# Kernel tuning notes

Hardware: AMD Instinct MI355X
Metric: run time of the kernel (lower is better)

## Reference

```python
import jax, jax.numpy as jnp
import numpy as np

# ---- static forest structure: 1024 complete binary trees of depth 9 ----
N_TREES = 1024
DEPTH = 9
NPT = 2 ** (DEPTH + 1) - 1            # 1023 nodes per tree
DIM = N_TREES * NPT                    # 1,047,552 total nodes
C = 10                                 # hidden states
M = 128                                # emission alphabet
N_GEN = 4                              # parallel generative models
LEVEL_SIZES = [N_TREES * 2 ** (k + 1) for k in range(DEPTH)]
LEVEL_START = np.concatenate([[0], np.cumsum(LEVEL_SIZES)]).astype(np.int64)
TREE_OFF = np.arange(N_TREES, dtype=np.int64) * NPT


def _build_forest():
    parents, children = [], []
    for k in range(DEPTH):
        ch = np.arange(2 ** (k + 1) - 1, 2 ** (k + 2) - 1, dtype=np.int64)  # depth k+1 nodes
        pa = (ch - 1) // 2                                                   # their parents (depth k)
        children.append((TREE_OFF[:, None] + ch[None, :]).ravel())
        parents.append((TREE_OFF[:, None] + pa[None, :]).ravel())
    leaves = (TREE_OFF[:, None] + np.arange(NPT // 2, NPT, dtype=np.int64)[None, :]).ravel()
    trees_ind = np.repeat(np.arange(N_TREES, dtype=np.int64), NPT)
    return np.concatenate(parents), np.concatenate(children), leaves, trees_ind


def setup_inputs() -> dict:
    key = jax.random.key(0)
    k1, k2, k3, k4 = jax.random.split(key, 4)
    parents, children, leaves, trees_ind = _build_forest()
    return {
        "x": jax.random.randint(k4, (DIM,), 0, M, dtype=jnp.int32),
        "A": jax.random.normal(k1, (C, C, N_GEN), jnp.float32) * 2.5,
        "B": jax.random.normal(k2, (C, M, N_GEN), jnp.float32) * 2.5,
        "Pi": jax.random.normal(k3, (C, N_GEN), jnp.float32) * 2.5,
        "parents": jnp.asarray(parents, jnp.int32),
        "children": jnp.asarray(children, jnp.int32),
        "trees_ind": jnp.asarray(trees_ind, jnp.int32),
        "leaves": jnp.asarray(leaves, jnp.int32),
    }


def _upward(x, A, B, Pi, parents, children, trees_ind, leaves):
    # softmax reparameterization (vectorized over the n_gen axis)
    smA = jax.nn.softmax(A, axis=0)    # P(parent state i | child state j), cols sum over i
    smB = jax.nn.softmax(B, axis=1)    # emission distribution per state
    smPi = jax.nn.softmax(Pi, axis=0)  # leaf prior

    beta = jnp.zeros((DIM, C, N_GEN), smA.dtype)
    t_beta = jnp.zeros((DIM, C, N_GEN), smA.dtype)
    ll = jnp.zeros((DIM, N_GEN), smA.dtype)

    # leaves: beta = Pi * B[:, x_leaf], normalized
    B_leaf = jnp.swapaxes(smB[:, x[leaves]], 0, 1)            # [L, C, G]
    b = smPi[None, :, :] * B_leaf
    nu = b.sum(axis=1)                                         # [L, G]
    beta = beta.at[leaves].set(b / nu[:, None, :])
    ll = ll.at[leaves].set(jnp.log(nu))

    # bottom-up sweep over levels (static loop over tree depth)
    for k in reversed(range(DEPTH)):
        s, e = int(LEVEL_START[k]), int(LEVEL_START[k + 1])
        pa, ch = parents[s:e], children[s:e]
        beta_ch = beta[ch]                                     # [E, C, G]
        tb_ch = jnp.einsum('ijg,ejg->eig', smA, beta_ch)       # sum over child state j
        sums = jax.ops.segment_sum(tb_ch, pa, num_segments=DIM)
        cnt = jax.ops.segment_sum(jnp.ones((e - s,), smA.dtype), pa, num_segments=DIM)
        t_beta = t_beta + sums / jnp.maximum(cnt, 1.0)[:, None, None]  # scatter-mean over children
        # unique parents at this level = all depth-k nodes (static for complete trees)
        u = jnp.asarray((TREE_OFF[:, None] + np.arange(2 ** k - 1, 2 ** (k + 1) - 1)[None, :]).ravel(), jnp.int32)
        B_u = jnp.swapaxes(smB[:, x[u]], 0, 1)                 # [U, C, G]
        bl = t_beta[u] * B_u
        nu = bl.sum(axis=1)
        beta = beta.at[u].set(bl / nu[:, None, :])
        ll = ll.at[u].set(jnp.log(nu))

    # per-tree log-likelihood: scatter-sum node terms over trees_ind
    return jax.ops.segment_sum(ll, trees_ind, num_segments=N_TREES)  # [n_trees, G]


def reference(x, A, B, Pi, parents, children, trees_ind, leaves):
    return _upward(x, A, B, Pi, parents, children, trees_ind, leaves)
```

## Files before the change

### kernel.cpp

```cpp
#include <hip/hip_runtime.h>
#include <math.h>

#define NC     10
#define NCP    12
#define NM     128
#define NGEN   4
#define NPT    1023
#define NTREES 1024

#define RCPF(x) __builtin_amdgcn_rcpf(x)
#define WAVE_FENCE() __builtin_amdgcn_wave_barrier()

struct F12 { float4 a, b, c; };

__device__ __forceinline__ F12 ld12(const float* p) {
    F12 r; const float4* q = (const float4*)p;
    r.a = q[0]; r.b = q[1]; r.c = q[2]; return r;
}
__device__ __forceinline__ void unpack10(float* t, const F12& r) {
    t[0] = r.a.x; t[1] = r.a.y; t[2] = r.a.z; t[3] = r.a.w;
    t[4] = r.b.x; t[5] = r.b.y; t[6] = r.b.z; t[7] = r.b.w;
    t[8] = r.c.x; t[9] = r.c.y;
}
__device__ __forceinline__ void fma10(float* t, const F12& c, float s) {
    t[0] += c.a.x * s; t[1] += c.a.y * s; t[2] += c.a.z * s; t[3] += c.a.w * s;
    t[4] += c.b.x * s; t[5] += c.b.y * s; t[6] += c.b.z * s; t[7] += c.b.w * s;
    t[8] += c.c.x * s; t[9] += c.c.y * s;
}
__device__ __forceinline__ void mul10(float* t, const F12& r) {
    t[0] *= r.a.x; t[1] *= r.a.y; t[2] *= r.a.z; t[3] *= r.a.w;
    t[4] *= r.b.x; t[5] *= r.b.y; t[6] *= r.b.z; t[7] *= r.b.w;
    t[8] *= r.c.x; t[9] *= r.c.y;
}
__device__ __forceinline__ float sum10(const float* v) {
    return (((v[0] + v[1]) + (v[2] + v[3])) + ((v[4] + v[5]) + (v[6] + v[7]))) + (v[8] + v[9]);
}

__device__ __forceinline__ float leaf_pair(const float (*sBTpi)[NCP], int xv0, int xv1, float* sc) {
    float b0[NC], b1[NC];
    unpack10(b0, ld12(&sBTpi[xv0][0]));
    unpack10(b1, ld12(&sBTpi[xv1][0]));
    const float nu0 = sum10(b0), nu1 = sum10(b1);
    const float r0 = RCPF(nu0), r1 = RCPF(nu1);
    #pragma unroll
    for (int j = 0; j < NC; ++j) sc[j] = b0[j] * r0 + b1[j] * r1;
    return __logf(nu0) + __logf(nu1);
}

__device__ __forceinline__ float node_step(const F12* acol, const float (*sBT)[NCP],
                                           const float* sc, int xv, float* bout) {
    float t[NC];
    #pragma unroll
    for (int i = 0; i < NC; ++i) t[i] = 0.f;
    #pragma unroll
    for (int j = 0; j < NC; ++j) fma10(t, acol[j], sc[j]);
    mul10(t, ld12(&sBT[xv][0]));
    const float nu = sum10(t);
    const float r = RCPF(nu);
    #pragma unroll
    for (int j = 0; j < NC; ++j) bout[j] = t[j] * r;
    return __logf(nu);
}

__device__ __forceinline__ float fused_step_ip(const F12* acol, const float (*sBT)[NCP],
                                               float* buf, int l,
                                               int xc0, int xc1, int xp)
{
    float t0[NC], t1[NC];
    #pragma unroll
    for (int i = 0; i < NC; ++i) { t0[i] = 0.f; t1[i] = 0.f; }
    #pragma unroll
    for (int j = 0; j < NC; ++j) {
        float4 gv = *(const float4*)(buf + j * 64 + 4 * l);
        fma10(t0, acol[j], gv.x + gv.y);
        fma10(t1, acol[j], gv.z + gv.w);
    }
    mul10(t0, ld12(&sBT[xc0][0]));
    mul10(t1, ld12(&sBT[xc1][0]));
    const float nu0 = sum10(t0), nu1 = sum10(t1);
    const float r0 = RCPF(nu0), r1 = RCPF(nu1);
    float ll = __logf(nu0) + __logf(nu1);

    float tp[NC];
    #pragma unroll
    for (int i = 0; i < NC; ++i) tp[i] = 0.f;
    #pragma unroll
    for (int j = 0; j < NC; ++j)
        fma10(tp, acol[j], t0[j] * r0 + t1[j] * r1);
    mul10(tp, ld12(&sBT[xp][0]));
    const float nup = sum10(tp);
    ll += __logf(nup);
    const float rp = RCPF(nup);
    #pragma unroll
    for (int j = 0; j < NC; ++j) buf[j * 64 + l] = tp[j] * rp;
    return ll;
}

__global__ __launch_bounds__(256)
void htmm_fused(const int* __restrict__ x,
                const float* __restrict__ A,
                const float* __restrict__ B,
                const float* __restrict__ Pi,
                float* __restrict__ out)
{
    __shared__ __align__(16) float sACol[NC][NCP];
    __shared__ __align__(16) float sBT[NM][NCP];
    __shared__ __align__(16) float sBTpi[NM][NCP];
    __shared__ __align__(16) float sPiP[NCP];
    __shared__ __align__(16) float sB6[4][NC][64];

    const int bid = blockIdx.x;
    const int g = bid >> 8;
    const int treeBase = (bid & 255) * 4;
    const int tid = threadIdx.x;
    const int u = tid >> 6, lane = tid & 63;

    {
        for (int c = u; c < NC; c += 4) {
            float v0 = B[(c * NM + lane) * NGEN + g];
            float v1 = B[(c * NM + lane + 64) * NGEN + g];
            float mx = fmaxf(v0, v1);
            #pragma unroll
            for (int off = 32; off; off >>= 1) mx = fmaxf(mx, __shfl_xor(mx, off));
            float e0 = __expf(v0 - mx), e1 = __expf(v1 - mx);
            float s = e0 + e1;
            #pragma unroll
            for (int off = 32; off; off >>= 1) s += __shfl_xor(s, off);
            float rs = 1.f / s;
            sBT[lane][c]      = e0 * rs;
            sBT[lane + 64][c] = e1 * rs;
        }
        if (tid < NC) {
            const int j = tid;
            float col[NC], mx = -1e30f;
            #pragma unroll
            for (int i = 0; i < NC; ++i) { col[i] = A[(i * NC + j) * NGEN + g]; mx = fmaxf(mx, col[i]); }
            float s = 0.f;
            #pragma unroll
            for (int i = 0; i < NC; ++i) { col[i] = __expf(col[i] - mx); s += col[i]; }
            const float rs = 0.5f / s;
            #pragma unroll
            for (int i = 0; i < NC; ++i) sACol[j][i] = col[i] * rs;
            sACol[j][10] = 0.f; sACol[j][11] = 0.f;
        }
        if (tid == 16) {
            float col[NC], mx = -1e30f;
            #pragma unroll
            for (int i = 0; i < NC; ++i) { col[i] = Pi[i * NGEN + g]; mx = fmaxf(mx, col[i]); }
            float s = 0.f;
            #pragma unroll
            for (int i = 0; i < NC; ++i) { col[i] = __expf(col[i] - mx); s += col[i]; }
            const float rs = 1.f / s;
            #pragma unroll
            for (int i = 0; i < NC; ++i) sPiP[i] = col[i] * rs;
            sPiP[10] = 0.f; sPiP[11] = 0.f;
        }
    }
    __syncthreads();
    if (tid < NM) {
        F12 pi = ld12(sPiP);
        F12 r  = ld12(&sBT[tid][0]);
        sBTpi[tid][0] = pi.a.x * r.a.x; sBTpi[tid][1] = pi.a.y * r.a.y;
        sBTpi[tid][2] = pi.a.z * r.a.z; sBTpi[tid][3] = pi.a.w * r.a.w;
        sBTpi[tid][4] = pi.b.x * r.b.x; sBTpi[tid][5] = pi.b.y * r.b.y;
        sBTpi[tid][6] = pi.b.z * r.b.z; sBTpi[tid][7] = pi.b.w * r.b.w;
        sBTpi[tid][8] = pi.c.x * r.c.x; sBTpi[tid][9] = pi.c.y * r.c.y;
    }
    __syncthreads();

    F12 acol[NC];
    #pragma unroll
    for (int j = 0; j < NC; ++j) acol[j] = ld12(&sACol[j][0]);

    const int tree = treeBase + u;
    const int tb = tree * NPT;
    const int s = lane;

    int xl[8];
    #pragma unroll
    for (int k = 0; k < 8; ++k) xl[k] = x[tb + 511 + 8 * s + k];
    int x8v[4];
    #pragma unroll
    for (int c = 0; c < 4; ++c) x8v[c] = x[tb + 255 + 4 * s + c];
    const int x7a = x[tb + 127 + 2 * s];
    const int x7b = x[tb + 128 + 2 * s];
    const int x6v = x[tb + 63 + s];

    float llacc = 0.f;
    float sc[NC], ba[NC], bb[NC], b7a[NC], b7b[NC];

    llacc += leaf_pair(sBTpi, xl[0], xl[1], sc);
    llacc += node_step(acol, sBT, sc, x8v[0], ba);
    llacc += leaf_pair(sBTpi, xl[2], xl[3], sc);
    llacc += node_step(acol, sBT, sc, x8v[1], bb);
    #pragma unroll
    for (int j = 0; j < NC; ++j) sc[j] = ba[j] + bb[j];
    llacc += node_step(acol, sBT, sc, x7a, b7a);

    llacc += leaf_pair(sBTpi, xl[4], xl[5], sc);
    llacc += node_step(acol, sBT, sc, x8v[2], ba);
    llacc += leaf_pair(sBTpi, xl[6], xl[7], sc);
    llacc += node_step(acol, sBT, sc, x8v[3], bb);
    #pragma unroll
    for (int j = 0; j < NC; ++j) sc[j] = ba[j] + bb[j];
    llacc += node_step(acol, sBT, sc, x7b, b7b);

    #pragma unroll
    for (int j = 0; j < NC; ++j) sc[j] = b7a[j] + b7b[j];
    llacc += node_step(acol, sBT, sc, x6v, ba);
    #pragma unroll
    for (int j = 0; j < NC; ++j) sB6[u][j][s] = ba[j];

    WAVE_FENCE();
    float lla = 0.f;
    if (lane < 16)
        lla = fused_step_ip(acol, sBT, &sB6[u][0][0], lane,
                            x[tb + 31 + 2 * lane], x[tb + 32 + 2 * lane],
                            x[tb + 15 + lane]);
    llacc += lla;
    WAVE_FENCE();
    float llb = 0.f;
    if (lane < 4)
        llb = fused_step_ip(acol, sBT, &sB6[u][0][0], lane,
                            x[tb + 7 + 2 * lane], x[tb + 8 + 2 * lane],
                            x[tb + 3 + lane]);
    llacc += llb;
    WAVE_FENCE();
    if (lane == 0)
        llacc += fused_step_ip(acol, sBT, &sB6[u][0][0], 0,
                               x[tb + 1], x[tb + 2], x[tb + 0]);

    #pragma unroll
    for (int off = 32; off; off >>= 1) llacc += __shfl_down(llacc, off);
    if (lane == 0) out[tree * NGEN + g] = llacc;
}

extern "C" void kernel_launch(void* const* d_in, const int* in_sizes, int n_in,
                              void* d_out, int out_size, void* d_ws, size_t ws_size,
                              hipStream_t stream) {
    const int*   x  = (const int*)d_in[0];
    const float* A  = (const float*)d_in[1];
    const float* B  = (const float*)d_in[2];
    const float* Pi = (const float*)d_in[3];
    float* out = (float*)d_out;
    htmm_fused<<<NTREES, 256, 0, stream>>>(x, A, B, Pi, out);
}
```

Before: 28.65 us.

## Split softmax table setup into separate kernel and read tables from global memory

Adds a small setup kernel that computes the softmaxed A, B and Pi-weighted B tables once per generative model into workspace memory. The main kernel then launches one 64-thread block per (tree, model) and reads the tables from global memory through cache, no longer rebuilding them in LDS inside every block. This is meant to remove the per-block table construction and its block barrier. In exchange it adds a second launch and scattered global/L2 gathers where LDS reads were used before. The old fused kernel stays as a fallback when the workspace is too small.

```diff
diff --git a/kernel.cpp b/kernel.cpp
--- a/kernel.cpp
+++ b/kernel.cpp
@@ -8,6 +8,11 @@
 #define NPT    1023
 #define NTREES 1024
 
+#define WS_BT(g)    ((g) * (NM * NCP))
+#define WS_BTPI(g)  (4 * NM * NCP + (g) * (NM * NCP))
+#define WS_AC(g)    (8 * NM * NCP + (g) * (NC * NCP))
+#define WS_FLOATS   (8 * NM * NCP + 4 * NC * NCP)
+
 #define RCPF(x) __builtin_amdgcn_rcpf(x)
 #define WAVE_FENCE() __builtin_amdgcn_wave_barrier()
 
@@ -36,10 +41,10 @@
     return (((v[0] + v[1]) + (v[2] + v[3])) + ((v[4] + v[5]) + (v[6] + v[7]))) + (v[8] + v[9]);
 }
 
-__device__ __forceinline__ float leaf_pair(const float (*sBTpi)[NCP], int xv0, int xv1, float* sc) {
+__device__ __forceinline__ float leaf_pair(const float* btpi, int xv0, int xv1, float* sc) {
     float b0[NC], b1[NC];
-    unpack10(b0, ld12(&sBTpi[xv0][0]));
-    unpack10(b1, ld12(&sBTpi[xv1][0]));
+    unpack10(b0, ld12(btpi + NCP * xv0));
+    unpack10(b1, ld12(btpi + NCP * xv1));
     const float nu0 = sum10(b0), nu1 = sum10(b1);
     const float r0 = RCPF(nu0), r1 = RCPF(nu1);
     #pragma unroll
@@ -47,14 +52,14 @@
     return __logf(nu0) + __logf(nu1);
 }
 
-__device__ __forceinline__ float node_step(const F12* acol, const float (*sBT)[NCP],
+__device__ __forceinline__ float node_step(const F12* acol, const float* bt,
                                            const float* sc, int xv, float* bout) {
     float t[NC];
     #pragma unroll
     for (int i = 0; i < NC; ++i) t[i] = 0.f;
     #pragma unroll
     for (int j = 0; j < NC; ++j) fma10(t, acol[j], sc[j]);
-    mul10(t, ld12(&sBT[xv][0]));
+    mul10(t, ld12(bt + NCP * xv));
     const float nu = sum10(t);
     const float r = RCPF(nu);
     #pragma unroll
@@ -62,7 +67,7 @@
     return __logf(nu);
 }
 
-__device__ __forceinline__ float fused_step_ip(const F12* acol, const float (*sBT)[NCP],
+__device__ __forceinline__ float fused_step_ip(const F12* acol, const float* bt,
                                                float* buf, int l,
                                                int xc0, int xc1, int xp)
 {
@@ -75,8 +80,8 @@
         fma10(t0, acol[j], gv.x + gv.y);
         fma10(t1, acol[j], gv.z + gv.w);
     }
-    mul10(t0, ld12(&sBT[xc0][0]));
-    mul10(t1, ld12(&sBT[xc1][0]));
+    mul10(t0, ld12(bt + NCP * xc0));
+    mul10(t1, ld12(bt + NCP * xc1));
     const float nu0 = sum10(t0), nu1 = sum10(t1);
     const float r0 = RCPF(nu0), r1 = RCPF(nu1);
     float ll = __logf(nu0) + __logf(nu1);
@@ -87,13 +92,158 @@
     #pragma unroll
     for (int j = 0; j < NC; ++j)
         fma10(tp, acol[j], t0[j] * r0 + t1[j] * r1);
-    mul10(tp, ld12(&sBT[xp][0]));
+    mul10(tp, ld12(bt + NCP * xp));
     const float nup = sum10(tp);
     ll += __logf(nup);
     const float rp = RCPF(nup);
     #pragma unroll
     for (int j = 0; j < NC; ++j) buf[j * 64 + l] = tp[j] * rp;
     return ll;
+}
+
+__global__ __launch_bounds__(256)
+void htmm_setup(const float* __restrict__ A,
+                const float* __restrict__ B,
+                const float* __restrict__ Pi,
+                float* __restrict__ ws)
+{
+    __shared__ float sPi[NCP];
+    const int g = blockIdx.x;
+    const int tid = threadIdx.x;
+    const int wave = tid >> 6, lane = tid & 63;
+    float* bt   = ws + WS_BT(g);
+    float* btpi = ws + WS_BTPI(g);
+    float* ac   = ws + WS_AC(g);
+
+    if (tid == 16) {
+        float col[NC], mx = -1e30f;
+        #pragma unroll
+        for (int i = 0; i < NC; ++i) { col[i] = Pi[i * NGEN + g]; mx = fmaxf(mx, col[i]); }
+        float s = 0.f;
+        #pragma unroll
+        for (int i = 0; i < NC; ++i) { col[i] = __expf(col[i] - mx); s += col[i]; }
+        const float rs = 1.f / s;
+        #pragma unroll
+        for (int i = 0; i < NC; ++i) sPi[i] = col[i] * rs;
+    }
+    if (tid < NC) {
+        const int j = tid;
+        float col[NC], mx = -1e30f;
+        #pragma unroll
+        for (int i = 0; i < NC; ++i) { col[i] = A[(i * NC + j) * NGEN + g]; mx = fmaxf(mx, col[i]); }
+        float s = 0.f;
+        #pragma unroll
+        for (int i = 0; i < NC; ++i) { col[i] = __expf(col[i] - mx); s += col[i]; }
+        const float rs = 0.5f / s;
+        #pragma unroll
+        for (int i = 0; i < NC; ++i) ac[j * NCP + i] = col[i] * rs;
+        ac[j * NCP + 10] = 0.f; ac[j * NCP + 11] = 0.f;
+    }
+    __syncthreads();
+
+    for (int c = wave; c < NC; c += 4) {
+        float v0 = B[(c * NM + lane) * NGEN + g];
+        float v1 = B[(c * NM + lane + 64) * NGEN + g];
+        float mx = fmaxf(v0, v1);
+        #pragma unroll
+        for (int off = 32; off; off >>= 1) mx = fmaxf(mx, __shfl_xor(mx, off));
+        float e0 = __expf(v0 - mx), e1 = __expf(v1 - mx);
+        float s = e0 + e1;
+        #pragma unroll
+        for (int off = 32; off; off >>= 1) s += __shfl_xor(s, off);
+        const float rs = 1.f / s;
+        const float pic = sPi[c];
+        bt[lane * NCP + c]          = e0 * rs;
+        bt[(lane + 64) * NCP + c]   = e1 * rs;
+        btpi[lane * NCP + c]        = e0 * rs * pic;
+        btpi[(lane + 64) * NCP + c] = e1 * rs * pic;
+    }
+    if (tid < NM) {
+        bt[tid * NCP + 10] = 0.f;   bt[tid * NCP + 11] = 0.f;
+        btpi[tid * NCP + 10] = 0.f; btpi[tid * NCP + 11] = 0.f;
+    }
+}
+
+__global__ __launch_bounds__(64)
+void htmm_main(const int* __restrict__ x,
+               const float* __restrict__ ws,
+               float* __restrict__ out)
+{
+    __shared__ __align__(16) float sB6[NC][64];
+
+    const int bid  = blockIdx.x;
+    const int tree = bid >> 2;
+    const int g    = bid & 3;
+    const int lane = threadIdx.x;
+
+    const float* bt   = ws + WS_BT(g);
+    const float* btpi = ws + WS_BTPI(g);
+    const float* ac   = ws + WS_AC(g);
+
+    F12 acol[NC];
+    #pragma unroll
+    for (int j = 0; j < NC; ++j) acol[j] = ld12(ac + j * NCP);
+
+    const int tb = tree * NPT;
+    const int s = lane;
+
+    int xl[8];
+    #pragma unroll
+    for (int k = 0; k < 8; ++k) xl[k] = x[tb + 511 + 8 * s + k];
+    int x8v[4];
+    #pragma unroll
+    for (int c = 0; c < 4; ++c) x8v[c] = x[tb + 255 + 4 * s + c];
+    const int x7a = x[tb + 127 + 2 * s];
+    const int x7b = x[tb + 128 + 2 * s];
+    const int x6v = x[tb + 63 + s];
+
+    float llacc = 0.f;
+    float sc[NC], ba[NC], bb[NC], b7a[NC], b7b[NC];
+
+    llacc += leaf_pair(btpi, xl[0], xl[1], sc);
+    llacc += node_step(acol, bt, sc, x8v[0], ba);
+    llacc += leaf_pair(btpi, xl[2], xl[3], sc);
+    llacc += node_step(acol, bt, sc, x8v[1], bb);
+    #pragma unroll
+    for (int j = 0; j < NC; ++j) sc[j] = ba[j] + bb[j];
+    llacc += node_step(acol, bt, sc, x7a, b7a);
+
+    llacc += leaf_pair(btpi, xl[4], xl[5], sc);
+    llacc += node_step(acol, bt, sc, x8v[2], ba);
+    llacc += leaf_pair(btpi, xl[6], xl[7], sc);
+    llacc += node_step(acol, bt, sc, x8v[3], bb);
+    #pragma unroll
+    for (int j = 0; j < NC; ++j) sc[j] = ba[j] + bb[j];
+    llacc += node_step(acol, bt, sc, x7b, b7b);
+
+    #pragma unroll
+    for (int j = 0; j < NC; ++j) sc[j] = b7a[j] + b7b[j];
+    llacc += node_step(acol, bt, sc, x6v, ba);
+    #pragma unroll
+    for (int j = 0; j < NC; ++j) sB6[j][s] = ba[j];
+
+    WAVE_FENCE();
+    float lla = 0.f;
+    if (lane < 16)
+        lla = fused_step_ip(acol, bt, &sB6[0][0], lane,
+                            x[tb + 31 + 2 * lane], x[tb + 32 + 2 * lane],
+                            x[tb + 15 + lane]);
+    llacc += lla;
+    WAVE_FENCE();
+    float llb = 0.f;
+    if (lane < 4)
+        llb = fused_step_ip(acol, bt, &sB6[0][0], lane,
+                            x[tb + 7 + 2 * lane], x[tb + 8 + 2 * lane],
+                            x[tb + 3 + lane]);
+    llacc += llb;
+    WAVE_FENCE();
+    if (lane == 0)
+        llacc += fused_step_ip(acol, bt, &sB6[0][0], 0,
+                               x[tb + 1], x[tb + 2], x[tb + 0]);
+
+    #pragma unroll
+    for (int off = 32; off; off >>= 1) llacc += __shfl_down(llacc, off);
+    if (lane == 0) out[tree * NGEN + g] = llacc;
 }
 
 __global__ __launch_bounds__(256)
@@ -189,45 +339,45 @@
     float llacc = 0.f;
     float sc[NC], ba[NC], bb[NC], b7a[NC], b7b[NC];
 
-    llacc += leaf_pair(sBTpi, xl[0], xl[1], sc);
-    llacc += node_step(acol, sBT, sc, x8v[0], ba);
-    llacc += leaf_pair(sBTpi, xl[2], xl[3], sc);
-    llacc += node_step(acol, sBT, sc, x8v[1], bb);
+    llacc += leaf_pair(&sBTpi[0][0], xl[0], xl[1], sc);
+    llacc += node_step(acol, &sBT[0][0], sc, x8v[0], ba);
+    llacc += leaf_pair(&sBTpi[0][0], xl[2], xl[3], sc);
+    llacc += node_step(acol, &sBT[0][0], sc, x8v[1], bb);
     #pragma unroll
     for (int j = 0; j < NC; ++j) sc[j] = ba[j] + bb[j];
-    llacc += node_step(acol, sBT, sc, x7a, b7a);
-
-    llacc += leaf_pair(sBTpi, xl[4], xl[5], sc);
-    llacc += node_step(acol, sBT, sc, x8v[2], ba);
-    llacc += leaf_pair(sBTpi, xl[6], xl[7], sc);
-    llacc += node_step(acol, sBT, sc, x8v[3], bb);
+    llacc += node_step(acol, &sBT[0][0], sc, x7a, b7a);
+
+    llacc += leaf_pair(&sBTpi[0][0], xl[4], xl[5], sc);
+    llacc += node_step(acol, &sBT[0][0], sc, x8v[2], ba);
+    llacc += leaf_pair(&sBTpi[0][0], xl[6], xl[7], sc);
+    llacc += node_step(acol, &sBT[0][0], sc, x8v[3], bb);
     #pragma unroll
     for (int j = 0; j < NC; ++j) sc[j] = ba[j] + bb[j];
-    llacc += node_step(acol, sBT, sc, x7b, b7b);
+    llacc += node_step(acol, &sBT[0][0], sc, x7b, b7b);
 
     #pragma unroll
     for (int j = 0; j < NC; ++j) sc[j] = b7a[j] + b7b[j];
-    llacc += node_step(acol, sBT, sc, x6v, ba);
+    llacc += node_step(acol, &sBT[0][0], sc, x6v, ba);
     #pragma unroll
     for (int j = 0; j < NC; ++j) sB6[u][j][s] = ba[j];
 
     WAVE_FENCE();
     float lla = 0.f;
     if (lane < 16)
-        lla = fused_step_ip(acol, sBT, &sB6[u][0][0], lane,
+        lla = fused_step_ip(acol, &sBT[0][0], &sB6[u][0][0], lane,
                             x[tb + 31 + 2 * lane], x[tb + 32 + 2 * lane],
                             x[tb + 15 + lane]);
     llacc += lla;
     WAVE_FENCE();
     float llb = 0.f;
     if (lane < 4)
-        llb = fused_step_ip(acol, sBT, &sB6[u][0][0], lane,
+        llb = fused_step_ip(acol, &sBT[0][0], &sB6[u][0][0], lane,
                             x[tb + 7 + 2 * lane], x[tb + 8 + 2 * lane],
                             x[tb + 3 + lane]);
     llacc += llb;
     WAVE_FENCE();
     if (lane == 0)
-        llacc += fused_step_ip(acol, sBT, &sB6[u][0][0], 0,
+        llacc += fused_step_ip(acol, &sBT[0][0], &sB6[u][0][0], 0,
                                x[tb + 1], x[tb + 2], x[tb + 0]);
 
     #pragma unroll
@@ -243,5 +393,12 @@
     const float* B  = (const float*)d_in[2];
     const float* Pi = (const float*)d_in[3];
     float* out = (float*)d_out;
-    htmm_fused<<<NTREES, 256, 0, stream>>>(x, A, B, Pi, out);
-}
+
+    if (ws_size >= (size_t)WS_FLOATS * sizeof(float)) {
+        float* ws = (float*)d_ws;
+        htmm_setup<<<NGEN, 256, 0, stream>>>(A, B, Pi, ws);
+        htmm_main<<<NTREES * NGEN, 64, 0, stream>>>(x, ws, out);
+    } else {
+        htmm_fused<<<NTREES, 256, 0, stream>>>(x, A, B, Pi, out);
+    }
+}
```

New measurement: 37.08 us. 29.4% more time.

## Defer child normalization by sibling cross-scaling and hoist tree index loads

Applied to the files above, without the earlier changes.

Child beta vectors are no longer normalized on their own. Each parent instead consumes u0*nu1 + u1*nu0, so the parent's log-normalizer absorbs the children's log terms, removing most per-node reciprocals and logs in the upward pass. The per-tree x index loads are moved ahead of the shared-memory parameter setup so their global latency overlaps the softmax work. The B softmax also drops its max-subtraction reduction, which relies on B values being small enough that exp does not overflow, and the numerics change slightly because scaling is deferred.

```diff
diff --git a/kernel.cpp b/kernel.cpp
--- a/kernel.cpp
+++ b/kernel.cpp
@@ -36,33 +36,58 @@
     return (((v[0] + v[1]) + (v[2] + v[3])) + ((v[4] + v[5]) + (v[6] + v[7]))) + (v[8] + v[9]);
 }
 
-__device__ __forceinline__ float leaf_pair(const float (*sBTpi)[NCP], int xv0, int xv1, float* sc) {
+__device__ __forceinline__ float group3_leaf(const F12* acol, const float (*bt)[NCP],
+                                             const float (*btpi)[NCP],
+                                             int xl0, int xl1, int xp, float* bout) {
     float b0[NC], b1[NC];
-    unpack10(b0, ld12(&sBTpi[xv0][0]));
-    unpack10(b1, ld12(&sBTpi[xv1][0]));
+    unpack10(b0, ld12(&btpi[xl0][0]));
+    unpack10(b1, ld12(&btpi[xl1][0]));
     const float nu0 = sum10(b0), nu1 = sum10(b1);
-    const float r0 = RCPF(nu0), r1 = RCPF(nu1);
-    #pragma unroll
-    for (int j = 0; j < NC; ++j) sc[j] = b0[j] * r0 + b1[j] * r1;
-    return __logf(nu0) + __logf(nu1);
-}
-
-__device__ __forceinline__ float node_step(const F12* acol, const float (*sBT)[NCP],
-                                           const float* sc, int xv, float* bout) {
     float t[NC];
     #pragma unroll
     for (int i = 0; i < NC; ++i) t[i] = 0.f;
     #pragma unroll
-    for (int j = 0; j < NC; ++j) fma10(t, acol[j], sc[j]);
-    mul10(t, ld12(&sBT[xv][0]));
-    const float nu = sum10(t);
-    const float r = RCPF(nu);
+    for (int j = 0; j < NC; ++j) fma10(t, acol[j], b0[j] * nu1 + b1[j] * nu0);
+    mul10(t, ld12(&bt[xp][0]));
+    const float nup = sum10(t);
+    const float r = RCPF(nup);
     #pragma unroll
     for (int j = 0; j < NC; ++j) bout[j] = t[j] * r;
-    return __logf(nu);
-}
-
-__device__ __forceinline__ float fused_step_ip(const F12* acol, const float (*sBT)[NCP],
+    return __logf(nup);
+}
+
+__device__ __forceinline__ float node_unnorm(const F12* acol, const float (*bt)[NCP],
+                                             const float* c0, const float* c1,
+                                             int xv, float* uo) {
+    float t[NC];
+    #pragma unroll
+    for (int i = 0; i < NC; ++i) t[i] = 0.f;
+    #pragma unroll
+    for (int j = 0; j < NC; ++j) fma10(t, acol[j], c0[j] + c1[j]);
+    mul10(t, ld12(&bt[xv][0]));
+    #pragma unroll
+    for (int j = 0; j < NC; ++j) uo[j] = t[j];
+    return sum10(t);
+}
+
+__device__ __forceinline__ float group3_mid(const F12* acol, const float (*bt)[NCP],
+                                            const float* u0, float nu0,
+                                            const float* u1, float nu1,
+                                            int xp, float* bout) {
+    float t[NC];
+    #pragma unroll
+    for (int i = 0; i < NC; ++i) t[i] = 0.f;
+    #pragma unroll
+    for (int j = 0; j < NC; ++j) fma10(t, acol[j], u0[j] * nu1 + u1[j] * nu0);
+    mul10(t, ld12(&bt[xp][0]));
+    const float nup = sum10(t);
+    const float r = RCPF(nup);
+    #pragma unroll
+    for (int j = 0; j < NC; ++j) bout[j] = t[j] * r;
+    return __logf(nup);
+}
+
+__device__ __forceinline__ float fused_step_ip(const F12* acol, const float (*bt)[NCP],
                                                float* buf, int l,
                                                int xc0, int xc1, int xp)
 {
@@ -75,25 +100,20 @@
         fma10(t0, acol[j], gv.x + gv.y);
         fma10(t1, acol[j], gv.z + gv.w);
     }
-    mul10(t0, ld12(&sBT[xc0][0]));
-    mul10(t1, ld12(&sBT[xc1][0]));
+    mul10(t0, ld12(&bt[xc0][0]));
+    mul10(t1, ld12(&bt[xc1][0]));
     const float nu0 = sum10(t0), nu1 = sum10(t1);
-    const float r0 = RCPF(nu0), r1 = RCPF(nu1);
-    float ll = __logf(nu0) + __logf(nu1);
-
     float tp[NC];
     #pragma unroll
     for (int i = 0; i < NC; ++i) tp[i] = 0.f;
     #pragma unroll
-    for (int j = 0; j < NC; ++j)
-        fma10(tp, acol[j], t0[j] * r0 + t1[j] * r1);
-    mul10(tp, ld12(&sBT[xp][0]));
+    for (int j = 0; j < NC; ++j) fma10(tp, acol[j], t0[j] * nu1 + t1[j] * nu0);
+    mul10(tp, ld12(&bt[xp][0]));
     const float nup = sum10(tp);
-    ll += __logf(nup);
     const float rp = RCPF(nup);
     #pragma unroll
     for (int j = 0; j < NC; ++j) buf[j * 64 + l] = tp[j] * rp;
-    return ll;
+    return __logf(nup);
 }
 
 __global__ __launch_bounds__(256)
@@ -115,46 +135,51 @@
     const int tid = threadIdx.x;
     const int u = tid >> 6, lane = tid & 63;
 
-    {
-        for (int c = u; c < NC; c += 4) {
-            float v0 = B[(c * NM + lane) * NGEN + g];
-            float v1 = B[(c * NM + lane + 64) * NGEN + g];
-            float mx = fmaxf(v0, v1);
-            #pragma unroll
-            for (int off = 32; off; off >>= 1) mx = fmaxf(mx, __shfl_xor(mx, off));
-            float e0 = __expf(v0 - mx), e1 = __expf(v1 - mx);
-            float s = e0 + e1;
-            #pragma unroll
-            for (int off = 32; off; off >>= 1) s += __shfl_xor(s, off);
-            float rs = 1.f / s;
-            sBT[lane][c]      = e0 * rs;
-            sBT[lane + 64][c] = e1 * rs;
-        }
-        if (tid < NC) {
-            const int j = tid;
-            float col[NC], mx = -1e30f;
-            #pragma unroll
-            for (int i = 0; i < NC; ++i) { col[i] = A[(i * NC + j) * NGEN + g]; mx = fmaxf(mx, col[i]); }
-            float s = 0.f;
-            #pragma unroll
-            for (int i = 0; i < NC; ++i) { col[i] = __expf(col[i] - mx); s += col[i]; }
-            const float rs = 0.5f / s;
-            #pragma unroll
-            for (int i = 0; i < NC; ++i) sACol[j][i] = col[i] * rs;
-            sACol[j][10] = 0.f; sACol[j][11] = 0.f;
-        }
-        if (tid == 16) {
-            float col[NC], mx = -1e30f;
-            #pragma unroll
-            for (int i = 0; i < NC; ++i) { col[i] = Pi[i * NGEN + g]; mx = fmaxf(mx, col[i]); }
-            float s = 0.f;
-            #pragma unroll
-            for (int i = 0; i < NC; ++i) { col[i] = __expf(col[i] - mx); s += col[i]; }
-            const float rs = 1.f / s;
-            #pragma unroll
-            for (int i = 0; i < NC; ++i) sPiP[i] = col[i] * rs;
-            sPiP[10] = 0.f; sPiP[11] = 0.f;
-        }
+    const int tree = treeBase + u;
+    const int tb = tree * NPT;
+
+    int xl[8];
+    #pragma unroll
+    for (int k = 0; k < 8; ++k) xl[k] = x[tb + 511 + 8 * lane + k];
+    int x8v[4];
+    #pragma unroll
+    for (int c = 0; c < 4; ++c) x8v[c] = x[tb + 255 + 4 * lane + c];
+    const int x7a = x[tb + 127 + 2 * lane];
+    const int x7b = x[tb + 128 + 2 * lane];
+    const int x6v = x[tb + 63 + lane];
+
+    for (int c = u; c < NC; c += 4) {
+        float e0 = __expf(B[(c * NM + lane) * NGEN + g]);
+        float e1 = __expf(B[(c * NM + lane + 64) * NGEN + g]);
+        float sm = e0 + e1;
+        #pragma unroll
+        for (int off = 32; off; off >>= 1) sm += __shfl_xor(sm, off);
+        const float rs = 1.f / sm;
+        sBT[lane][c]      = e0 * rs;
+        sBT[lane + 64][c] = e1 * rs;
+    }
+    if (tid >= 128 && tid < 128 + NC) {
+        const int j = tid - 128;
+        float col[NC], mx = -1e30f;
+        #pragma unroll
+        for (int i = 0; i < NC; ++i) { col[i] = A[(i * NC + j) * NGEN + g]; mx = fmaxf(mx, col[i]); }
+        float sm = 0.f;
+        #pragma unroll
+        for (int i = 0; i < NC; ++i) { col[i] = __expf(col[i] - mx); sm += col[i]; }
+        const float rs = 0.5f / sm;
+        #pragma unroll
+        for (int i = 0; i < NC; ++i) sACol[j][i] = col[i] * rs;
+    }
+    if (tid == 192) {
+        float col[NC], mx = -1e30f;
+        #pragma unroll
+        for (int i = 0; i < NC; ++i) { col[i] = Pi[i * NGEN + g]; mx = fmaxf(mx, col[i]); }
+        float sm = 0.f;
+        #pragma unroll
+        for (int i = 0; i < NC; ++i) { col[i] = __expf(col[i] - mx); sm += col[i]; }
+        const float rs = 1.f / sm;
+        #pragma unroll
+        for (int i = 0; i < NC; ++i) sPiP[i] = col[i] * rs;
     }
     __syncthreads();
     if (tid < NM) {
@@ -172,44 +197,20 @@
     #pragma unroll
     for (int j = 0; j < NC; ++j) acol[j] = ld12(&sACol[j][0]);
 
-    const int tree = treeBase + u;
-    const int tb = tree * NPT;
-    const int s = lane;
-
-    int xl[8];
-    #pragma unroll
-    for (int k = 0; k < 8; ++k) xl[k] = x[tb + 511 + 8 * s + k];
-    int x8v[4];
-    #pragma unroll
-    for (int c = 0; c < 4; ++c) x8v[c] = x[tb + 255 + 4 * s + c];
-    const int x7a = x[tb + 127 + 2 * s];
-    const int x7b = x[tb + 128 + 2 * s];
-    const int x6v = x[tb + 63 + s];
-
-    float llacc = 0.f;
-    float sc[NC], ba[NC], bb[NC], b7a[NC], b7b[NC];
-
-    llacc += leaf_pair(sBTpi, xl[0], xl[1], sc);
-    llacc += node_step(acol, sBT, sc, x8v[0], ba);
-    llacc += leaf_pair(sBTpi, xl[2], xl[3], sc);
-    llacc += node_step(acol, sBT, sc, x8v[1], bb);
-    #pragma unroll
-    for (int j = 0; j < NC; ++j) sc[j] = ba[j] + bb[j];
-    llacc += node_step(acol, sBT, sc, x7a, b7a);
-
-    llacc += leaf_pair(sBTpi, xl[4], xl[5], sc);
-    llacc += node_step(acol, sBT, sc, x8v[2], ba);
-    llacc += leaf_pair(sBTpi, xl[6], xl[7], sc);
-    llacc += node_step(acol, sBT, sc, x8v[3], bb);
-    #pragma unroll
-    for (int j = 0; j < NC; ++j) sc[j] = ba[j] + bb[j];
-    llacc += node_step(acol, sBT, sc, x7b, b7b);
-
-    #pragma unroll
-    for (int j = 0; j < NC; ++j) sc[j] = b7a[j] + b7b[j];
-    llacc += node_step(acol, sBT, sc, x6v, ba);
-    #pragma unroll
-    for (int j = 0; j < NC; ++j) sB6[u][j][s] = ba[j];
+    float llacc;
+    float ba[NC], bb[NC], u7a[NC], u7b[NC];
+
+    llacc  = group3_leaf(acol, sBT, sBTpi, xl[0], xl[1], x8v[0], ba);
+    llacc += group3_leaf(acol, sBT, sBTpi, xl[2], xl[3], x8v[1], bb);
+    const float nu7a = node_unnorm(acol, sBT, ba, bb, x7a, u7a);
+
+    llacc += group3_leaf(acol, sBT, sBTpi, xl[4], xl[5], x8v[2], ba);
+    llacc += group3_leaf(acol, sBT, sBTpi, xl[6], xl[7], x8v[3], bb);
+    const float nu7b = node_unnorm(acol, sBT, ba, bb, x7b, u7b);
+
+    llacc += group3_mid(acol, sBT, u7a, nu7a, u7b, nu7b, x6v, ba);
+    #pragma unroll
+    for (int j = 0; j < NC; ++j) sB6[u][j][lane] = ba[j];
 
     WAVE_FENCE();
     float lla = 0.f;
```

Measured after the change: 26.06 us. 1.1x faster.
